# Kernel tuning notes

Hardware: AMD Instinct MI355X
Metric: run time of the kernel (lower is better)

The kernel has to match this reference:

```python
import jax, jax.numpy as jnp
import numpy as np

N = 16384          # num nodes
E = 262144         # num edges (before self loops)
IN_DIM = 128
HID = 128
OUT = 2
TRIM = 0.1
MAX_DEG = 48       # padded max in-degree (incl. self loop); safe bound for Poisson(16)+1
BN_EPS = 1e-5


def _lin_params(key, fan_in, fan_out):
    kw, kb = jax.random.split(key)
    s = 1.0 / np.sqrt(fan_in)
    W = jax.random.uniform(kw, (fan_in, fan_out), jnp.float32, -s, s)
    b = jax.random.uniform(kb, (fan_out,), jnp.float32, -s, s)
    return W, b


def setup_inputs() -> dict:
    key = jax.random.key(0)
    ks = jax.random.split(key, 8)
    x = jax.random.normal(ks[0], (N, IN_DIM), jnp.float32)
    edge_index = jax.random.randint(ks[1], (2, E), 0, N, jnp.int32)
    Wl0, bl0 = _lin_params(ks[2], IN_DIM, HID)
    Wr0, br0 = _lin_params(ks[3], IN_DIM, HID)
    Wl1, bl1 = _lin_params(ks[4], HID, HID)
    Wr1, br1 = _lin_params(ks[5], HID, HID)
    Wl2, bl2 = _lin_params(ks[6], HID, OUT)
    Wr2, br2 = _lin_params(ks[7], HID, OUT)
    g0 = jnp.ones((HID,), jnp.float32); be0 = jnp.zeros((HID,), jnp.float32)
    g1 = jnp.ones((HID,), jnp.float32); be1 = jnp.zeros((HID,), jnp.float32)
    return dict(x=x, edge_index=edge_index,
                Wl0=Wl0, bl0=bl0, Wr0=Wr0, br0=br0, g0=g0, be0=be0,
                Wl1=Wl1, bl1=bl1, Wr1=Wr1, br1=br1, g1=g1, be1=be1,
                Wl2=Wl2, bl2=bl2, Wr2=Wr2, br2=br2)


def _forward(edge_index, x, Wl0, bl0, Wr0, br0, g0, be0,
             Wl1, bl1, Wr1, br1, g1, be1, Wl2, bl2, Wr2, br2):
    loops = jnp.arange(N, dtype=edge_index.dtype)
    row = jnp.concatenate([edge_index[0], loops])   # source nodes
    col = jnp.concatenate([edge_index[1], loops])   # destination nodes
    counts = jax.ops.segment_sum(jnp.ones_like(col), col, num_segments=N)  # in-degree, int
    deg = jnp.maximum(counts, 1).astype(x.dtype)
    norm = 1.0 / deg[col]                            # 1/deg(dst), per edge

    # Edge ordering grouped by destination node; rank = slot within the node's group.
    perm = jnp.argsort(col, stable=True)
    col_s = col[perm]
    starts = jnp.cumsum(counts) - counts
    rank = jnp.arange(col.shape[0], dtype=counts.dtype) - starts[col_s]
    node_id = jnp.where(rank < MAX_DEG, col_s, N)    # overflow slots -> OOB, dropped by scatter

    t = jnp.maximum(1, jnp.floor(counts.astype(jnp.float32) * TRIM).astype(counts.dtype))
    tcnt = counts - 2 * t
    pos = jnp.arange(MAX_DEG)[None, :]
    sel = (pos >= t[:, None]) & (pos < (counts - t)[:, None])   # [N, MAX_DEG]
    use_trim = (counts >= 5) & (tcnt > 0)
    inv_tcnt = 1.0 / jnp.maximum(tcnt, 1).astype(x.dtype)

    def trimmed_scatter(msg):
        # plain mean fallback
        mean = jax.ops.segment_sum(msg, col, num_segments=N) / deg[:, None]
        d = msg.shape[1]
        # padded per-node buffer; +inf pads sort to the end (never selected by `sel`)
        dense = jnp.full((N, MAX_DEG, d), jnp.inf, msg.dtype)
        dense = dense.at[node_id, rank].set(msg[perm], mode='drop')
        sdense = jnp.sort(dense, axis=1)             # per-feature sort within each node
        tmean = jnp.sum(jnp.where(sel[:, :, None], sdense, 0.0), axis=1) * inv_tcnt[:, None]
        return jnp.where(use_trim[:, None], tmean, mean)

    def conv(h, Wl, bl, Wr, br):
        msg = (h @ Wl + bl)[row] * norm[:, None]
        return trimmed_scatter(msg) + h @ Wr + br

    bn_scale = jnp.float32(1.0 / np.sqrt(1.0 + BN_EPS))  # eval-mode BN: running mean 0, var 1
    h = conv(x, Wl0, bl0, Wr0, br0)
    h = jax.nn.relu(h * bn_scale * g0 + be0)
    h = conv(h, Wl1, bl1, Wr1, br1)
    h = jax.nn.relu(h * bn_scale * g1 + be1)
    return conv(h, Wl2, bl2, Wr2, br2)


def reference(x, edge_index, Wl0, bl0, Wr0, br0, g0, be0,
              Wl1, bl1, Wr1, br1, g1, be1, Wl2, bl2, Wr2, br2):
    return _forward(edge_index, x, Wl0, bl0, Wr0, br0, g0, be0,
                    Wl1, bl1, Wr1, br1, g1, be1, Wl2, bl2, Wr2, br2)
```

## Files before the change

### kernel.cpp

```cpp
#include <hip/hip_runtime.h>
#include <hip/hip_fp16.h>
#include <math.h>

#define GN    16384
#define MAXD  48
#define BN_SCALE 0.9999950000374998f

typedef __attribute__((ext_vector_type(8))) short short8;
typedef __attribute__((ext_vector_type(4))) float f32x4;
typedef _Float16 __attribute__((ext_vector_type(2))) h2v;

__device__ inline short f2bf(float x) {
    unsigned u = __float_as_uint(x);
    return (short)((u + 0x7fffu + ((u >> 16) & 1u)) >> 16);
}
__device__ inline float bf2f(short s) {
    return __uint_as_float(((unsigned)(unsigned short)s) << 16);
}

struct F2 { float x, y; };
__device__ inline F2 f2min(F2 a, F2 b) { return {fminf(a.x, b.x), fminf(a.y, b.y)}; }
__device__ inline F2 f2max(F2 a, F2 b) { return {fmaxf(a.x, b.x), fmaxf(a.y, b.y)}; }

__device__ inline F2 trim_core(const _Float16* __restrict__ HL,
                               const int* __restrict__ srow, int cnt, int d, int f2i)
{
    F2 tot = {0.f, 0.f};
    F2 s0 = { INFINITY,  INFINITY}, s1 = s0, s2 = s0, s3 = s0;
    F2 l0 = {-INFINITY, -INFINITY}, l1 = l0, l2 = l0, l3 = l0;

    if (cnt < 20) {
        for (int i = 0; i < d; ++i) {
            h2v hv = *reinterpret_cast<const h2v*>(HL + srow[i] + f2i);
            F2 x = {(float)hv[0], (float)hv[1]};
            tot.x += x.x; tot.y += x.y;
            s0 = f2min(s0, x);
            l0 = f2max(l0, x);
        }
    } else {
        for (int i = 0; i < d; ++i) {
            h2v hv = *reinterpret_cast<const h2v*>(HL + srow[i] + f2i);
            F2 x = {(float)hv[0], (float)hv[1]};
            tot.x += x.x; tot.y += x.y;
            F2 a = x;
            F2 t0 = f2min(s0, a); a = f2max(s0, a); s0 = t0;
            F2 t1 = f2min(s1, a); a = f2max(s1, a); s1 = t1;
            F2 t2 = f2min(s2, a); a = f2max(s2, a); s2 = t2;
            s3 = f2min(s3, a);
            F2 b = x;
            F2 u0 = f2max(l0, b); b = f2min(l0, b); l0 = u0;
            F2 u1 = f2max(l1, b); b = f2min(l1, b); l1 = u1;
            F2 u2 = f2max(l2, b); b = f2min(l2, b); l2 = u2;
            l3 = f2max(l3, b);
        }
    }

    int t = (int)floorf((float)cnt * 0.1f);
    if (t < 1) t = 1;
    int tcnt = cnt - 2 * t;
    bool use_trim = (cnt >= 5) && (tcnt > 0);
    float dd = (float)cnt;
    F2 res;
    if (use_trim) {
        int tt = min(t, 4);
        F2 bot = s0, top = l0;
        if (tt > 1) { bot.x += s1.x; bot.y += s1.y; top.x += l1.x; top.y += l1.y; }
        if (tt > 2) { bot.x += s2.x; bot.y += s2.y; top.x += l2.x; top.y += l2.y; }
        if (tt > 3) { bot.x += s3.x; bot.y += s3.y; top.x += l3.x; top.y += l3.y; }
        float inv = 1.0f / (dd * (float)tcnt);
        res.x = (tot.x - bot.x - top.x) * inv;
        res.y = (tot.y - bot.y - top.y) * inv;
    } else {
        float inv = 1.0f / (dd * dd);
        res.x = tot.x * inv;
        res.y = tot.y * inv;
    }
    return res;
}

__global__ __launch_bounds__(256) void k_prep(
    int* __restrict__ fill,
    const float* __restrict__ Wl0, const float* __restrict__ Wr0,
    const float* __restrict__ Wl1, const float* __restrict__ Wr1,
    short* __restrict__ W5)
{
    int t = blockIdx.x * 256 + threadIdx.x;
    fill[t] = 0;

    int layer = t >> 13;
    int g     = t & 8191;
    int split = (g >> 12) & 1;
    int ks    = (g >> 10) & 3;
    int nt    = (g >> 6) & 15;
    int l     = g & 63;
    int q = l >> 4, r = l & 15;
    int n = nt * 16 + r;
    const float* W = (n < 128) ? (layer ? Wl1 : Wl0) : (layer ? Wr1 : Wr0);
    int ncol = n & 127;
    short8 o8;
    #pragma unroll
    for (int j = 0; j < 8; ++j) {
        int k = ks * 32 + (j >> 2) * 16 + q * 4 + (j & 3);
        float wv = W[k * 128 + ncol];
        short hi = f2bf(wv);
        o8[j] = split ? f2bf(wv - bf2f(hi)) : hi;
    }
    *reinterpret_cast<short8*>(W5 + ((size_t)layer * 8192 + g) * 8) = o8;
}

__device__ inline void gemm_tile(const short8 Ahi[4], const short8 Alo[4],
                                 const short* __restrict__ W5,
                                 const float* __restrict__ bl,
                                 const float* __restrict__ br,
                                 _Float16* __restrict__ HL, float* __restrict__ HR,
                                 int tile, int half, int nhalf, int q, int r, int l)
{
    const float* bias = nhalf ? br : bl;
    f32x4 acc[8];
    #pragma unroll
    for (int nt = 0; nt < 8; ++nt) {
        float b = bias[nt * 16 + r];
        acc[nt] = (f32x4){b, b, b, b};
    }
    #pragma unroll
    for (int ks = 0; ks < 4; ++ks) {
        #pragma unroll
        for (int nt = 0; nt < 8; ++nt) {
            int ntg = nhalf * 8 + nt;
            short8 Bhi = *reinterpret_cast<const short8*>(
                W5 + ((size_t)(ks * 16 + ntg) * 64 + l) * 8);
            short8 Blo = *reinterpret_cast<const short8*>(
                W5 + ((size_t)((4 + ks) * 16 + ntg) * 64 + l) * 8);
            acc[nt] = __builtin_amdgcn_mfma_f32_16x16x32_bf16(Ahi[ks], Bhi, acc[nt], 0, 0, 0);
            acc[nt] = __builtin_amdgcn_mfma_f32_16x16x32_bf16(Ahi[ks], Blo, acc[nt], 0, 0, 0);
            acc[nt] = __builtin_amdgcn_mfma_f32_16x16x32_bf16(Alo[ks], Bhi, acc[nt], 0, 0, 0);
        }
    }
    const int rb = tile * 32 + half * 16 + 4 * q;
    if (nhalf == 0) {
        #pragma unroll
        for (int nt = 0; nt < 8; ++nt) {
            int c = nt * 16 + r;
            #pragma unroll
            for (int j = 0; j < 4; ++j)
                HL[(size_t)(rb + j) * 128 + c] = (_Float16)acc[nt][j];
        }
    } else {
        #pragma unroll
        for (int nt = 0; nt < 8; ++nt) {
            int c = nt * 16 + r;
            #pragma unroll
            for (int j = 0; j < 4; ++j)
                HR[(size_t)(rb + j) * 128 + c] = acc[nt][j];
        }
    }
}

__global__ __launch_bounds__(256) void k_fused0(
    const float* __restrict__ X, const int* __restrict__ ei, int E,
    int* __restrict__ adj, int* __restrict__ fill,
    const short* __restrict__ W5,
    const float* __restrict__ bl, const float* __restrict__ br,
    _Float16* __restrict__ HL, float* __restrict__ HR)
{
    const int tid = threadIdx.x;
    if (blockIdx.x >= 512) {
        const int* src = ei;
        const int* dst = ei + E;
        int g0 = (blockIdx.x - 512) * 256 + tid;
        for (int i = g0; i < E + GN; i += 128 * 256) {
            int s, dv;
            if (i < E) { s = src[i]; dv = dst[i]; }
            else       { s = i - E;  dv = i - E; }
            int slot = atomicAdd(&fill[dv], 1);
            if (slot < MAXD) adj[dv * MAXD + slot] = s;
        }
        return;
    }
    const int w = tid >> 6, l = tid & 63;
    const int q = l >> 4, r = l & 15;
    const int half = w & 1, nhalf = w >> 1;
    const int rowA = blockIdx.x * 32 + half * 16 + r;

    short8 Ahi[4], Alo[4];
    const float4* xp = reinterpret_cast<const float4*>(X + (size_t)rowA * 128);
    #pragma unroll
    for (int h = 0; h < 8; ++h) {
        float4 v = xp[h * 4 + q];
        float xv[4] = {v.x, v.y, v.z, v.w};
        int ks = h >> 1, hk = h & 1;
        #pragma unroll
        for (int j = 0; j < 4; ++j) {
            short hi = f2bf(xv[j]);
            Ahi[ks][hk * 4 + j] = hi;
            Alo[ks][hk * 4 + j] = f2bf(xv[j] - bf2f(hi));
        }
    }
    gemm_tile(Ahi, Alo, W5, bl, br, HL, HR, blockIdx.x, half, nhalf, q, r, l);
}

__global__ __launch_bounds__(256) void k_fused1(
    const _Float16* __restrict__ HL0, const float* __restrict__ HR0,
    const int* __restrict__ adj, const int* __restrict__ fill,
    const float* __restrict__ g, const float* __restrict__ be,
    const short* __restrict__ W5,
    const float* __restrict__ bl, const float* __restrict__ br,
    _Float16* __restrict__ HL1, float* __restrict__ HR1)
{
    __shared__ float hbs[32][132];
    __shared__ int sadj[4][MAXD];
    const int tid = threadIdx.x, w = tid >> 6, l = tid & 63;
    const int f2i = l * 2;
    const int v0 = blockIdx.x * 32;

    for (int s = 0; s < 8; ++s) {
        const int v = v0 + w * 8 + s;
        const int cnt = fill[v];
        const int d = min(cnt, MAXD);
        if (l < d) sadj[w][l] = adj[v * MAXD + l] * 128;
        F2 res = trim_core(HL0, sadj[w], cnt, d, f2i);
        const float2 hrv = *reinterpret_cast<const float2*>(HR0 + (size_t)v * 128 + f2i);
        hbs[w * 8 + s][f2i]     = fmaxf((res.x + hrv.x) * (BN_SCALE * g[f2i])     + be[f2i],     0.f);
        hbs[w * 8 + s][f2i + 1] = fmaxf((res.y + hrv.y) * (BN_SCALE * g[f2i + 1]) + be[f2i + 1], 0.f);
    }
    __syncthreads();

    const int q = l >> 4, r = l & 15;
    const int half = w & 1, nhalf = w >> 1;
    const int m = half * 16 + r;
    short8 Ahi[4], Alo[4];
    #pragma unroll
    for (int h = 0; h < 8; ++h) {
        float4 vv = *reinterpret_cast<const float4*>(&hbs[m][h * 16 + 4 * q]);
        float xv[4] = {vv.x, vv.y, vv.z, vv.w};
        int ks = h >> 1, hk = h & 1;
        #pragma unroll
        for (int j = 0; j < 4; ++j) {
            short hi = f2bf(xv[j]);
            Ahi[ks][hk * 4 + j] = hi;
            Alo[ks][hk * 4 + j] = f2bf(xv[j] - bf2f(hi));
        }
    }
    gemm_tile(Ahi, Alo, W5, bl, br, HL1, HR1, blockIdx.x, half, nhalf, q, r, l);
}

__global__ __launch_bounds__(256) void k_fused2(
    const _Float16* __restrict__ HL1, const float* __restrict__ HR1,
    const int* __restrict__ adj, const int* __restrict__ fill,
    const float* __restrict__ g, const float* __restrict__ be,
    const float* __restrict__ Wl2, const float* __restrict__ bl2,
    const float* __restrict__ Wr2, const float* __restrict__ br2,
    float* __restrict__ hl2, float* __restrict__ hr2)
{
    __shared__ int sadj[4][MAXD];
    const int tid = threadIdx.x, w = tid >> 6, l = tid & 63;
    const int f2i = l * 2;
    const int v = blockIdx.x * 4 + w;
    const int cnt = fill[v];
    const int d = min(cnt, MAXD);
    if (l < d) sadj[w][l] = adj[v * MAXD + l] * 128;
    F2 res = trim_core(HL1, sadj[w], cnt, d, f2i);
    const float2 hrv = *reinterpret_cast<const float2*>(HR1 + (size_t)v * 128 + f2i);
    float h0 = fmaxf((res.x + hrv.x) * (BN_SCALE * g[f2i])     + be[f2i],     0.f);
    float h1 = fmaxf((res.y + hrv.y) * (BN_SCALE * g[f2i + 1]) + be[f2i + 1], 0.f);

    float4 wl = *reinterpret_cast<const float4*>(Wl2 + l * 4);
    float4 wr = *reinterpret_cast<const float4*>(Wr2 + l * 4);
    float p0 = h0 * wl.x + h1 * wl.z;
    float p1 = h0 * wl.y + h1 * wl.w;
    float p2 = h0 * wr.x + h1 * wr.z;
    float p3 = h0 * wr.y + h1 * wr.w;
    #pragma unroll
    for (int off = 1; off < 64; off <<= 1) {
        p0 += __shfl_xor(p0, off);
        p1 += __shfl_xor(p1, off);
        p2 += __shfl_xor(p2, off);
        p3 += __shfl_xor(p3, off);
    }
    if (l == 0) {
        hl2[v * 2 + 0] = p0 + bl2[0];
        hl2[v * 2 + 1] = p1 + bl2[1];
        hr2[v * 2 + 0] = p2 + br2[0];
        hr2[v * 2 + 1] = p3 + br2[1];
    }
}

__global__ __launch_bounds__(256) void k_agg_out(
    const float* __restrict__ hl2, const float* __restrict__ hr2,
    const int* __restrict__ adj, const int* __restrict__ fill,
    float* __restrict__ out)
{
    int idx = blockIdx.x * 256 + threadIdx.x;
    int v = idx >> 1, j = idx & 1;
    int cnt = fill[v];
    int d = min(cnt, MAXD);
    const int* ap = adj + v * MAXD;

    float total = 0.f;
    float s0 = INFINITY, s1 = INFINITY, s2 = INFINITY, s3 = INFINITY;
    float l0 = -INFINITY, l1 = -INFINITY, l2 = -INFINITY, l3 = -INFINITY;
    for (int i = 0; i < d; ++i) {
        float x = hl2[ap[i] * 2 + j];
        total += x;
        float a = x;
        float t0 = fminf(s0, a); a = fmaxf(s0, a); s0 = t0;
        float t1 = fminf(s1, a); a = fmaxf(s1, a); s1 = t1;
        float t2 = fminf(s2, a); a = fmaxf(s2, a); s2 = t2;
        s3 = fminf(s3, a);
        float b = x;
        float u0 = fmaxf(l0, b); b = fminf(l0, b); l0 = u0;
        float u1 = fmaxf(l1, b); b = fminf(l1, b); l1 = u1;
        float u2 = fmaxf(l2, b); b = fminf(l2, b); l2 = u2;
        l3 = fmaxf(l3, b);
    }

    int t = (int)floorf((float)cnt * 0.1f);
    if (t < 1) t = 1;
    int tcnt = cnt - 2 * t;
    bool use_trim = (cnt >= 5) && (tcnt > 0);
    float dd = (float)cnt;
    float res;
    if (use_trim) {
        int tt = min(t, 4);
        float bot = s0, top = l0;
        if (tt > 1) { bot += s1; top += l1; }
        if (tt > 2) { bot += s2; top += l2; }
        if (tt > 3) { bot += s3; top += l3; }
        res = (total - bot - top) / (dd * (float)tcnt);
    } else {
        res = total / (dd * dd);
    }
    out[idx] = res + hr2[idx];
}

extern "C" void kernel_launch(void* const* d_in, const int* in_sizes, int n_in,
                              void* d_out, int out_size, void* d_ws, size_t ws_size,
                              hipStream_t stream)
{
    const float* x   = (const float*)d_in[0];
    const int*   ei  = (const int*)d_in[1];
    const int    E   = in_sizes[1] / 2;
    const float* Wl0 = (const float*)d_in[2];
    const float* bl0 = (const float*)d_in[3];
    const float* Wr0 = (const float*)d_in[4];
    const float* br0 = (const float*)d_in[5];
    const float* g0  = (const float*)d_in[6];
    const float* be0 = (const float*)d_in[7];
    const float* Wl1 = (const float*)d_in[8];
    const float* bl1 = (const float*)d_in[9];
    const float* Wr1 = (const float*)d_in[10];
    const float* br1 = (const float*)d_in[11];
    const float* g1  = (const float*)d_in[12];
    const float* be1 = (const float*)d_in[13];
    const float* Wl2 = (const float*)d_in[14];
    const float* bl2 = (const float*)d_in[15];
    const float* Wr2 = (const float*)d_in[16];
    const float* br2 = (const float*)d_in[17];
    float* out = (float*)d_out;

    char* w = (char*)d_ws;
    int*      adj  = (int*)w;       w += (size_t)GN * MAXD * 4;
    int*      fill = (int*)w;       w += (size_t)GN * 4;
    _Float16* HL0  = (_Float16*)w;  w += (size_t)GN * 128 * 2;
    float*    HR0  = (float*)w;     w += (size_t)GN * 128 * 4;
    _Float16* HL1  = (_Float16*)w;  w += (size_t)GN * 128 * 2;
    float*    HR1  = (float*)w;     w += (size_t)GN * 128 * 4;
    short*    W5   = (short*)w;     w += (size_t)2 * 8192 * 16;
    float*    hl2  = (float*)w;     w += (size_t)GN * 2 * 4;
    float*    hr2  = (float*)w;     w += (size_t)GN * 2 * 4;

    k_prep  <<<GN / 256, 256, 0, stream>>>(fill, Wl0, Wr0, Wl1, Wr1, W5);
    k_fused0<<<640, 256, 0, stream>>>(x, ei, E, adj, fill, W5, bl0, br0, HL0, HR0);
    k_fused1<<<GN / 32, 256, 0, stream>>>(HL0, HR0, adj, fill, g0, be0,
                                          W5 + (size_t)8192 * 8, bl1, br1, HL1, HR1);
    k_fused2<<<GN / 4, 256, 0, stream>>>(HL1, HR1, adj, fill, g1, be1,
                                         Wl2, bl2, Wr2, br2, hl2, hr2);
    k_agg_out<<<GN * 2 / 256, 256, 0, stream>>>(hl2, hr2, adj, fill, out);
}
```

Baseline: 194.9 us.

## Batch neighbor gathers eightfold and use 512-thread blocks for fused GEMM kernels

The trimmed-mean aggregation loops now issue eight independent neighbor gathers before doing the min/max network, so more memory loads are in flight per thread. k_fused0 and k_fused1 move from 256-thread to 512-thread blocks. Each wave now computes a quarter of the output columns with a templated GEMM tile, and each wave in k_fused1 aggregates 4 nodes instead of 8. This is meant to hide gather latency and raise parallelism per tile, at the cost of more registers for the batched loads and larger blocks.

Result: faster. 179.0 us (-8.1%).

```diff
diff --git a/kernel.cpp b/kernel.cpp
--- a/kernel.cpp
+++ b/kernel.cpp
@@ -30,7 +30,21 @@
     F2 l0 = {-INFINITY, -INFINITY}, l1 = l0, l2 = l0, l3 = l0;
 
     if (cnt < 20) {
-        for (int i = 0; i < d; ++i) {
+        int i = 0;
+        for (; i + 8 <= d; i += 8) {
+            h2v b[8];
+            #pragma unroll
+            for (int k = 0; k < 8; ++k)
+                b[k] = *reinterpret_cast<const h2v*>(HL + srow[i + k] + f2i);
+            #pragma unroll
+            for (int k = 0; k < 8; ++k) {
+                F2 x = {(float)b[k][0], (float)b[k][1]};
+                tot.x += x.x; tot.y += x.y;
+                s0 = f2min(s0, x);
+                l0 = f2max(l0, x);
+            }
+        }
+        for (; i < d; ++i) {
             h2v hv = *reinterpret_cast<const h2v*>(HL + srow[i] + f2i);
             F2 x = {(float)hv[0], (float)hv[1]};
             tot.x += x.x; tot.y += x.y;
@@ -38,7 +52,29 @@
             l0 = f2max(l0, x);
         }
     } else {
-        for (int i = 0; i < d; ++i) {
+        int i = 0;
+        for (; i + 8 <= d; i += 8) {
+            h2v b[8];
+            #pragma unroll
+            for (int k = 0; k < 8; ++k)
+                b[k] = *reinterpret_cast<const h2v*>(HL + srow[i + k] + f2i);
+            #pragma unroll
+            for (int k = 0; k < 8; ++k) {
+                F2 x = {(float)b[k][0], (float)b[k][1]};
+                tot.x += x.x; tot.y += x.y;
+                F2 a = x;
+                F2 t0 = f2min(s0, a); a = f2max(s0, a); s0 = t0;
+                F2 t1 = f2min(s1, a); a = f2max(s1, a); s1 = t1;
+                F2 t2 = f2min(s2, a); a = f2max(s2, a); s2 = t2;
+                s3 = f2min(s3, a);
+                F2 bb = x;
+                F2 u0 = f2max(l0, bb); bb = f2min(l0, bb); l0 = u0;
+                F2 u1 = f2max(l1, bb); bb = f2min(l1, bb); l1 = u1;
+                F2 u2 = f2max(l2, bb); bb = f2min(l2, bb); l2 = u2;
+                l3 = f2max(l3, bb);
+            }
+        }
+        for (; i < d; ++i) {
             h2v hv = *reinterpret_cast<const h2v*>(HL + srow[i] + f2i);
             F2 x = {(float)hv[0], (float)hv[1]};
             tot.x += x.x; tot.y += x.y;
@@ -47,11 +83,11 @@
             F2 t1 = f2min(s1, a); a = f2max(s1, a); s1 = t1;
             F2 t2 = f2min(s2, a); a = f2max(s2, a); s2 = t2;
             s3 = f2min(s3, a);
-            F2 b = x;
-            F2 u0 = f2max(l0, b); b = f2min(l0, b); l0 = u0;
-            F2 u1 = f2max(l1, b); b = f2min(l1, b); l1 = u1;
-            F2 u2 = f2max(l2, b); b = f2min(l2, b); l2 = u2;
-            l3 = f2max(l3, b);
+            F2 bb = x;
+            F2 u0 = f2max(l0, bb); bb = f2min(l0, bb); l0 = u0;
+            F2 u1 = f2max(l1, bb); bb = f2min(l1, bb); l1 = u1;
+            F2 u2 = f2max(l2, bb); bb = f2min(l2, bb); l2 = u2;
+            l3 = f2max(l3, bb);
         }
     }
 
@@ -108,25 +144,26 @@
     *reinterpret_cast<short8*>(W5 + ((size_t)layer * 8192 + g) * 8) = o8;
 }
 
-__device__ inline void gemm_tile(const short8 Ahi[4], const short8 Alo[4],
-                                 const short* __restrict__ W5,
-                                 const float* __restrict__ bl,
-                                 const float* __restrict__ br,
-                                 _Float16* __restrict__ HL, float* __restrict__ HR,
-                                 int tile, int half, int nhalf, int q, int r, int l)
-{
-    const float* bias = nhalf ? br : bl;
-    f32x4 acc[8];
-    #pragma unroll
-    for (int nt = 0; nt < 8; ++nt) {
-        float b = bias[nt * 16 + r];
+template<int NT>
+__device__ inline void gemm_tile_t(const short8 Ahi[4], const short8 Alo[4],
+                                   const short* __restrict__ W5,
+                                   const float* __restrict__ bl,
+                                   const float* __restrict__ br,
+                                   _Float16* __restrict__ HL, float* __restrict__ HR,
+                                   int tile, int half, int ntg0, int q, int r, int l)
+{
+    f32x4 acc[NT];
+    #pragma unroll
+    for (int nt = 0; nt < NT; ++nt) {
+        int ntg = ntg0 + nt;
+        float b = (ntg < 8) ? bl[ntg * 16 + r] : br[(ntg - 8) * 16 + r];
         acc[nt] = (f32x4){b, b, b, b};
     }
     #pragma unroll
     for (int ks = 0; ks < 4; ++ks) {
         #pragma unroll
-        for (int nt = 0; nt < 8; ++nt) {
-            int ntg = nhalf * 8 + nt;
+        for (int nt = 0; nt < NT; ++nt) {
+            int ntg = ntg0 + nt;
             short8 Bhi = *reinterpret_cast<const short8*>(
                 W5 + ((size_t)(ks * 16 + ntg) * 64 + l) * 8);
             short8 Blo = *reinterpret_cast<const short8*>(
@@ -137,18 +174,16 @@
         }
     }
     const int rb = tile * 32 + half * 16 + 4 * q;
-    if (nhalf == 0) {
-        #pragma unroll
-        for (int nt = 0; nt < 8; ++nt) {
-            int c = nt * 16 + r;
+    #pragma unroll
+    for (int nt = 0; nt < NT; ++nt) {
+        int ntg = ntg0 + nt;
+        if (ntg < 8) {
+            int c = ntg * 16 + r;
             #pragma unroll
             for (int j = 0; j < 4; ++j)
                 HL[(size_t)(rb + j) * 128 + c] = (_Float16)acc[nt][j];
-        }
-    } else {
-        #pragma unroll
-        for (int nt = 0; nt < 8; ++nt) {
-            int c = nt * 16 + r;
+        } else {
+            int c = (ntg - 8) * 16 + r;
             #pragma unroll
             for (int j = 0; j < 4; ++j)
                 HR[(size_t)(rb + j) * 128 + c] = acc[nt][j];
@@ -156,7 +191,7 @@
     }
 }
 
-__global__ __launch_bounds__(256) void k_fused0(
+__global__ __launch_bounds__(512, 4) void k_fused0(
     const float* __restrict__ X, const int* __restrict__ ei, int E,
     int* __restrict__ adj, int* __restrict__ fill,
     const short* __restrict__ W5,
@@ -167,8 +202,8 @@
     if (blockIdx.x >= 512) {
         const int* src = ei;
         const int* dst = ei + E;
-        int g0 = (blockIdx.x - 512) * 256 + tid;
-        for (int i = g0; i < E + GN; i += 128 * 256) {
+        int g0 = (blockIdx.x - 512) * 512 + tid;
+        for (int i = g0; i < E + GN; i += 64 * 512) {
             int s, dv;
             if (i < E) { s = src[i]; dv = dst[i]; }
             else       { s = i - E;  dv = i - E; }
@@ -179,7 +214,7 @@
     }
     const int w = tid >> 6, l = tid & 63;
     const int q = l >> 4, r = l & 15;
-    const int half = w & 1, nhalf = w >> 1;
+    const int half = w & 1, quarter = w >> 1;
     const int rowA = blockIdx.x * 32 + half * 16 + r;
 
     short8 Ahi[4], Alo[4];
@@ -196,10 +231,10 @@
             Alo[ks][hk * 4 + j] = f2bf(xv[j] - bf2f(hi));
         }
     }
-    gemm_tile(Ahi, Alo, W5, bl, br, HL, HR, blockIdx.x, half, nhalf, q, r, l);
-}
-
-__global__ __launch_bounds__(256) void k_fused1(
+    gemm_tile_t<4>(Ahi, Alo, W5, bl, br, HL, HR, blockIdx.x, half, quarter * 4, q, r, l);
+}
+
+__global__ __launch_bounds__(512, 4) void k_fused1(
     const _Float16* __restrict__ HL0, const float* __restrict__ HR0,
     const int* __restrict__ adj, const int* __restrict__ fill,
     const float* __restrict__ g, const float* __restrict__ be,
@@ -208,25 +243,25 @@
     _Float16* __restrict__ HL1, float* __restrict__ HR1)
 {
     __shared__ float hbs[32][132];
-    __shared__ int sadj[4][MAXD];
+    __shared__ int sadj[8][MAXD];
     const int tid = threadIdx.x, w = tid >> 6, l = tid & 63;
     const int f2i = l * 2;
     const int v0 = blockIdx.x * 32;
 
-    for (int s = 0; s < 8; ++s) {
-        const int v = v0 + w * 8 + s;
+    for (int s = 0; s < 4; ++s) {
+        const int v = v0 + w * 4 + s;
         const int cnt = fill[v];
         const int d = min(cnt, MAXD);
         if (l < d) sadj[w][l] = adj[v * MAXD + l] * 128;
         F2 res = trim_core(HL0, sadj[w], cnt, d, f2i);
         const float2 hrv = *reinterpret_cast<const float2*>(HR0 + (size_t)v * 128 + f2i);
-        hbs[w * 8 + s][f2i]     = fmaxf((res.x + hrv.x) * (BN_SCALE * g[f2i])     + be[f2i],     0.f);
-        hbs[w * 8 + s][f2i + 1] = fmaxf((res.y + hrv.y) * (BN_SCALE * g[f2i + 1]) + be[f2i + 1], 0.f);
+        hbs[w * 4 + s][f2i]     = fmaxf((res.x + hrv.x) * (BN_SCALE * g[f2i])     + be[f2i],     0.f);
+        hbs[w * 4 + s][f2i + 1] = fmaxf((res.y + hrv.y) * (BN_SCALE * g[f2i + 1]) + be[f2i + 1], 0.f);
     }
     __syncthreads();
 
     const int q = l >> 4, r = l & 15;
-    const int half = w & 1, nhalf = w >> 1;
+    const int half = w & 1, quarter = w >> 1;
     const int m = half * 16 + r;
     short8 Ahi[4], Alo[4];
     #pragma unroll
@@ -241,7 +276,7 @@
             Alo[ks][hk * 4 + j] = f2bf(xv[j] - bf2f(hi));
         }
     }
-    gemm_tile(Ahi, Alo, W5, bl, br, HL1, HR1, blockIdx.x, half, nhalf, q, r, l);
+    gemm_tile_t<4>(Ahi, Alo, W5, bl, br, HL1, HR1, blockIdx.x, half, quarter * 4, q, r, l);
 }
 
 __global__ __launch_bounds__(256) void k_fused2(
@@ -299,7 +334,28 @@
     float total = 0.f;
     float s0 = INFINITY, s1 = INFINITY, s2 = INFINITY, s3 = INFINITY;
     float l0 = -INFINITY, l1 = -INFINITY, l2 = -INFINITY, l3 = -INFINITY;
-    for (int i = 0; i < d; ++i) {
+    int i = 0;
+    for (; i + 8 <= d; i += 8) {
+        float b[8];
+        #pragma unroll
+        for (int k = 0; k < 8; ++k) b[k] = hl2[ap[i + k] * 2 + j];
+        #pragma unroll
+        for (int k = 0; k < 8; ++k) {
+            float x = b[k];
+            total += x;
+            float a = x;
+            float t0 = fminf(s0, a); a = fmaxf(s0, a); s0 = t0;
+            float t1 = fminf(s1, a); a = fmaxf(s1, a); s1 = t1;
+            float t2 = fminf(s2, a); a = fmaxf(s2, a); s2 = t2;
+            s3 = fminf(s3, a);
+            float bb = x;
+            float u0 = fmaxf(l0, bb); bb = fminf(l0, bb); l0 = u0;
+            float u1 = fmaxf(l1, bb); bb = fminf(l1, bb); l1 = u1;
+            float u2 = fmaxf(l2, bb); bb = fminf(l2, bb); l2 = u2;
+            l3 = fmaxf(l3, bb);
+        }
+    }
+    for (; i < d; ++i) {
         float x = hl2[ap[i] * 2 + j];
         total += x;
         float a = x;
@@ -307,11 +363,11 @@
         float t1 = fminf(s1, a); a = fmaxf(s1, a); s1 = t1;
         float t2 = fminf(s2, a); a = fmaxf(s2, a); s2 = t2;
         s3 = fminf(s3, a);
-        float b = x;
-        float u0 = fmaxf(l0, b); b = fminf(l0, b); l0 = u0;
-        float u1 = fmaxf(l1, b); b = fminf(l1, b); l1 = u1;
-        float u2 = fmaxf(l2, b); b = fminf(l2, b); l2 = u2;
-        l3 = fmaxf(l3, b);
+        float bb = x;
+        float u0 = fmaxf(l0, bb); bb = fminf(l0, bb); l0 = u0;
+        float u1 = fmaxf(l1, bb); bb = fminf(l1, bb); l1 = u1;
+        float u2 = fmaxf(l2, bb); bb = fminf(l2, bb); l2 = u2;
+        l3 = fmaxf(l3, bb);
     }
 
     int t = (int)floorf((float)cnt * 0.1f);
@@ -370,8 +426,8 @@
     float*    hr2  = (float*)w;     w += (size_t)GN * 2 * 4;
 
     k_prep  <<<GN / 256, 256, 0, stream>>>(fill, Wl0, Wr0, Wl1, Wr1, W5);
-    k_fused0<<<640, 256, 0, stream>>>(x, ei, E, adj, fill, W5, bl0, br0, HL0, HR0);
-    k_fused1<<<GN / 32, 256, 0, stream>>>(HL0, HR0, adj, fill, g0, be0,
+    k_fused0<<<576, 512, 0, stream>>>(x, ei, E, adj, fill, W5, bl0, br0, HL0, HR0);
+    k_fused1<<<GN / 32, 512, 0, stream>>>(HL0, HR0, adj, fill, g0, be0,
                                           W5 + (size_t)8192 * 8, bl1, br1, HL1, HR1);
     k_fused2<<<GN / 4, 256, 0, stream>>>(HL1, HR1, adj, fill, g1, be1,
                                          Wl2, bl2, Wr2, br2, hl2, hr2);
```
